# Kernel tuning notes

Hardware: AMD Instinct MI355X
Metric: run time of the kernel (lower is better)

## Reference

```python
import jax, jax.numpy as jnp
import numpy as np

B, S, N, DIN, DOUT = 8, 2048, 16, 1024, 1024

def setup_inputs() -> dict:
    key = jax.random.key(0)
    k1, k2, k3, k4 = jax.random.split(key, 4)
    x = jax.random.normal(k1, (B, S, DIN), dtype=jnp.float32)
    # selection_probs: per-batch mixture weights over total_options (rows sum to 1)
    logits = jax.random.uniform(k2, (B, N), dtype=jnp.float32)
    selection_probs = jax.nn.softmax(logits, axis=-1)
    # kaiming_uniform(a=sqrt(5)) over fan_in=DIN -> bound = 1/sqrt(DIN)
    bound = 1.0 / np.sqrt(DIN)
    weight = jax.random.uniform(k3, (N, DOUT, DIN), dtype=jnp.float32, minval=-bound, maxval=bound)
    bias = jax.random.uniform(k4, (N, DOUT), dtype=jnp.float32, minval=-bound, maxval=bound)
    return {"x": x, "selection_probs": selection_probs, "weight": weight, "bias": bias}

def reference(x, selection_probs, weight, bias):
    # Math identical to: einsum('nij,baj->bani', W, x) then einsum('bani,bn->bai', ., p)
    # but mixes weights per-batch first (same contraction, avoids the [B,S,N,DOUT] tensor).
    mixed_w = jnp.einsum('bn,nij->bij', selection_probs, weight)   # [B, DOUT, DIN]
    out = jnp.einsum('bij,baj->bai', mixed_w, x)                   # [B, S, DOUT]
    mixed_b = jnp.einsum('bn,ni->bi', selection_probs, bias)       # [B, DOUT]
    return out + mixed_b[:, None, :]
```

## Files before the change

### kernel.cpp

```cpp
#include <hip/hip_runtime.h>
#include <hip/hip_bf16.h>
#include <stdint.h>

#define BB 8
#define SS 2048
#define NEXP 16
#define DIN 1024
#define DOUT 1024

typedef short bf16x8 __attribute__((ext_vector_type(8)));
typedef float floatx4 __attribute__((ext_vector_type(4)));

__device__ __forceinline__ unsigned short f2bf(float f) {
    union { float f; unsigned int u; } v; v.f = f;
    unsigned int u = v.u;
    unsigned int r = u + 0x7FFFu + ((u >> 16) & 1u);
    return (unsigned short)(r >> 16);
}

__device__ __forceinline__ void gload16(const void* g, void* l) {
    __builtin_amdgcn_global_load_lds(
        (const __attribute__((address_space(1))) void*)g,
        (__attribute__((address_space(3))) void*)l,
        16, 0, 0);
}

__global__ __launch_bounds__(256) void prep_kernel(
    const float* __restrict__ x, const float* __restrict__ p,
    const float* __restrict__ w, const float* __restrict__ bias,
    unsigned short* __restrict__ xb, unsigned short* __restrict__ mw,
    float* __restrict__ mb)
{
    const int tid = threadIdx.x;
    const int blk = blockIdx.x;

    if (blk < 8192) {
        const long gid = (long)blk * 256 + tid;
        const float4* xv = (const float4*)x;
        float4 v0 = xv[gid * 2 + 0];
        float4 v1 = xv[gid * 2 + 1];
        uint4 o;
        o.x = (unsigned)f2bf(v0.x) | ((unsigned)f2bf(v0.y) << 16);
        o.y = (unsigned)f2bf(v0.z) | ((unsigned)f2bf(v0.w) << 16);
        o.z = (unsigned)f2bf(v1.x) | ((unsigned)f2bf(v1.y) << 16);
        o.w = (unsigned)f2bf(v1.z) | ((unsigned)f2bf(v1.w) << 16);
        ((uint4*)xb)[gid] = o;
    } else if (blk < 9216) {
        __shared__ float sp[BB * NEXP];
        if (tid < BB * NEXP) sp[tid] = p[tid];
        __syncthreads();
        const long t  = (long)(blk - 8192) * 256 + tid;
        const long j4 = t * 4;
        float acc[BB][4];
        #pragma unroll
        for (int b = 0; b < BB; ++b)
            #pragma unroll
            for (int k = 0; k < 4; ++k) acc[b][k] = 0.f;
        #pragma unroll
        for (int n = 0; n < NEXP; ++n) {
            float4 wv = *(const float4*)(w + (long)n * DOUT * DIN + j4);
            #pragma unroll
            for (int b = 0; b < BB; ++b) {
                float pb = sp[b * NEXP + n];
                acc[b][0] += pb * wv.x; acc[b][1] += pb * wv.y;
                acc[b][2] += pb * wv.z; acc[b][3] += pb * wv.w;
            }
        }
        #pragma unroll
        for (int b = 0; b < BB; ++b) {
            uint2 o;
            o.x = (unsigned)f2bf(acc[b][0]) | ((unsigned)f2bf(acc[b][1]) << 16);
            o.y = (unsigned)f2bf(acc[b][2]) | ((unsigned)f2bf(acc[b][3]) << 16);
            *(uint2*)(mw + (long)b * DOUT * DIN + j4) = o;
        }
    } else {
        const long t = (long)(blk - 9216) * 256 + tid;
        const int b = (int)(t >> 10), i = (int)(t & 1023);
        float s = 0.f;
        #pragma unroll
        for (int n = 0; n < NEXP; ++n) s += p[b * NEXP + n] * bias[n * DOUT + i];
        mb[t] = s;
    }
}

__global__ __launch_bounds__(256) void gemm_kernel(
    const unsigned short* __restrict__ xb,
    const unsigned short* __restrict__ mw,
    const float* __restrict__ mb,
    float* __restrict__ out)
{
    __shared__ __align__(16) unsigned short sA[128 * 64];
    __shared__ __align__(16) unsigned short sB[128 * 64];

    const int tid  = threadIdx.x;
    const int wave = tid >> 6;
    const int lane = tid & 63;
    const int b    = blockIdx.x;
    const int tileN = blockIdx.y * 128;
    const int tileM = blockIdx.z * 128;

    const unsigned short* Ag = xb + (long)b * SS * DIN;
    const unsigned short* Bg = mw + (long)b * DOUT * DIN;

    const int q     = lane >> 4;
    const int r16   = lane & 15;
    const int mBase = 64 * (wave >> 1);
    const int nBase = 64 * (wave & 1);

    const int sRow   = lane >> 3;
    const int sColSw = (((lane & 7) ^ sRow) * 8);

    const unsigned short* aSrc[4]; const unsigned short* bSrc[4];
    unsigned short* aDst[4]; unsigned short* bDst[4];
    #pragma unroll
    for (int c = 0; c < 4; ++c) {
        const int chunk = wave * 4 + c;
        const int row   = chunk * 8 + sRow;
        aSrc[c] = Ag + (long)(tileM + row) * DIN + sColSw;
        bSrc[c] = Bg + (long)(tileN + row) * DIN + sColSw;
        aDst[c] = &sA[chunk * 512];
        bDst[c] = &sB[chunk * 512];
    }

    const int swz  = r16 & 7;
    const int colK0 = ((q)     ^ swz) * 8;
    const int colK1 = ((q + 4) ^ swz) * 8;

    floatx4 acc[4][4];
    #pragma unroll
    for (int mi = 0; mi < 4; ++mi)
        #pragma unroll
        for (int ni = 0; ni < 4; ++ni)
            acc[mi][ni] = (floatx4){0.f, 0.f, 0.f, 0.f};

    #pragma unroll
    for (int t = 0; t < 16; ++t) {
        __syncthreads();
        #pragma unroll
        for (int c = 0; c < 4; ++c) {
            gload16(aSrc[c] + 64 * t, aDst[c]);
            gload16(bSrc[c] + 64 * t, bDst[c]);
        }
        __syncthreads();

        #pragma unroll
        for (int kh = 0; kh < 2; ++kh) {
            const int col = kh ? colK1 : colK0;
            bf16x8 af[4], bfv[4];
            #pragma unroll
            for (int i = 0; i < 4; ++i)
                af[i] = *(const bf16x8*)&sA[(mBase + 16 * i + r16) * 64 + col];
            #pragma unroll
            for (int i = 0; i < 4; ++i)
                bfv[i] = *(const bf16x8*)&sB[(nBase + 16 * i + r16) * 64 + col];
            #pragma unroll
            for (int mi = 0; mi < 4; ++mi)
                #pragma unroll
                for (int ni = 0; ni < 4; ++ni)
                    acc[mi][ni] = __builtin_amdgcn_mfma_f32_16x16x32_bf16(
                        af[mi], bfv[ni], acc[mi][ni], 0, 0, 0);
        }
    }

    float bv[4];
    #pragma unroll
    for (int ni = 0; ni < 4; ++ni)
        bv[ni] = mb[b * DOUT + tileN + nBase + 16 * ni + r16];

    #pragma unroll
    for (int mi = 0; mi < 4; ++mi) {
        #pragma unroll
        for (int rr = 0; rr < 4; ++rr) {
            const int row = tileM + mBase + 16 * mi + q * 4 + rr;
            float* orow = out + (long)b * SS * DOUT + (long)row * DOUT;
            #pragma unroll
            for (int ni = 0; ni < 4; ++ni)
                orow[tileN + nBase + 16 * ni + r16] = acc[mi][ni][rr] + bv[ni];
        }
    }
}

extern "C" void kernel_launch(void* const* d_in, const int* in_sizes, int n_in,
                              void* d_out, int out_size, void* d_ws, size_t ws_size,
                              hipStream_t stream) {
    const float* x    = (const float*)d_in[0];
    const float* p    = (const float*)d_in[1];
    const float* w    = (const float*)d_in[2];
    const float* bias = (const float*)d_in[3];
    float* out = (float*)d_out;

    unsigned short* xb = (unsigned short*)d_ws;
    unsigned short* mw = (unsigned short*)((char*)d_ws + (size_t)33554432);
    float*          mb = (float*)((char*)d_ws + (size_t)33554432 + 16777216);

    prep_kernel<<<dim3(9248), 256, 0, stream>>>(x, p, w, bias, xb, mw, mb);

    dim3 ggrid(BB, DOUT / 128, SS / 128);
    gemm_kernel<<<ggrid, 256, 0, stream>>>(xb, mw, mb, out);
}
```

Baseline: 210.3 us.

## Merge x conversion and weight mixing into each prep block with interleaved order

The prep kernel drops from 9248 blocks to 1056. Each of the first 1024 blocks now converts a 4096-float4 slice of x to bf16 and also computes its weight-mix slice, with odd blocks doing the weight mix first, so memory-bound conversion and the FMA-heavy mixing overlap within and across blocks. The intent is to cut block launch overhead and the tail imbalance between the two phases. In exchange there are fewer blocks for latency hiding and longer per-block work.

Measured after the change: 222.1 us. +5.6%, slower.

```diff
diff --git a/kernel.cpp b/kernel.cpp
--- a/kernel.cpp
+++ b/kernel.cpp
@@ -34,22 +34,36 @@
     const int tid = threadIdx.x;
     const int blk = blockIdx.x;
 
-    if (blk < 8192) {
-        const long gid = (long)blk * 256 + tid;
+    if (blk >= 1024) {
+        const long t = (long)(blk - 1024) * 256 + tid;
+        const int b = (int)(t >> 10), i = (int)(t & 1023);
+        float s = 0.f;
+        #pragma unroll
+        for (int n = 0; n < NEXP; ++n) s += p[b * NEXP + n] * bias[n * DOUT + i];
+        mb[t] = s;
+        return;
+    }
+
+    __shared__ float sp[BB * NEXP];
+    if (tid < BB * NEXP) sp[tid] = p[tid];
+    __syncthreads();
+
+    auto xconv = [&]() {
         const float4* xv = (const float4*)x;
-        float4 v0 = xv[gid * 2 + 0];
-        float4 v1 = xv[gid * 2 + 1];
-        uint4 o;
-        o.x = (unsigned)f2bf(v0.x) | ((unsigned)f2bf(v0.y) << 16);
-        o.y = (unsigned)f2bf(v0.z) | ((unsigned)f2bf(v0.w) << 16);
-        o.z = (unsigned)f2bf(v1.x) | ((unsigned)f2bf(v1.y) << 16);
-        o.w = (unsigned)f2bf(v1.z) | ((unsigned)f2bf(v1.w) << 16);
-        ((uint4*)xb)[gid] = o;
-    } else if (blk < 9216) {
-        __shared__ float sp[BB * NEXP];
-        if (tid < BB * NEXP) sp[tid] = p[tid];
-        __syncthreads();
-        const long t  = (long)(blk - 8192) * 256 + tid;
+        uint2* xo = (uint2*)xb;
+        const int base = blk * 4096 + tid;
+        #pragma unroll
+        for (int u = 0; u < 16; ++u) {
+            float4 v = xv[base + u * 256];
+            uint2 o;
+            o.x = (unsigned)f2bf(v.x) | ((unsigned)f2bf(v.y) << 16);
+            o.y = (unsigned)f2bf(v.z) | ((unsigned)f2bf(v.w) << 16);
+            xo[base + u * 256] = o;
+        }
+    };
+
+    auto wmix = [&]() {
+        const long t  = (long)blk * 256 + tid;
         const long j4 = t * 4;
         float acc[BB][4];
         #pragma unroll
@@ -73,14 +87,10 @@
             o.y = (unsigned)f2bf(acc[b][2]) | ((unsigned)f2bf(acc[b][3]) << 16);
             *(uint2*)(mw + (long)b * DOUT * DIN + j4) = o;
         }
-    } else {
-        const long t = (long)(blk - 9216) * 256 + tid;
-        const int b = (int)(t >> 10), i = (int)(t & 1023);
-        float s = 0.f;
-        #pragma unroll
-        for (int n = 0; n < NEXP; ++n) s += p[b * NEXP + n] * bias[n * DOUT + i];
-        mb[t] = s;
-    }
+    };
+
+    if (blk & 1) { wmix(); xconv(); }
+    else         { xconv(); wmix(); }
 }
 
 __global__ __launch_bounds__(256) void gemm_kernel(
@@ -193,7 +203,7 @@
     unsigned short* mw = (unsigned short*)((char*)d_ws + (size_t)33554432);
     float*          mb = (float*)((char*)d_ws + (size_t)33554432 + 16777216);
 
-    prep_kernel<<<dim3(9248), 256, 0, stream>>>(x, p, w, bias, xb, mw, mb);
+    prep_kernel<<<dim3(1056), 256, 0, stream>>>(x, p, w, bias, xb, mw, mb);
 
     dim3 ggrid(BB, DOUT / 128, SS / 128);
     gemm_kernel<<<ggrid, 256, 0, stream>>>(xb, mw, mb, out);
```
